# Optimization experiments

Hardware: AMD Instinct MI355X
Metric: run time of the kernel (lower is better)

The kernel has to match this reference:

```python
import jax, jax.numpy as jnp
import numpy as np

BS, D, M = 64, 256, 512


def setup_inputs() -> dict:
    key = jax.random.key(0)
    ks = jax.random.split(key, 6)
    # Small scales keep the 10-step RLS recurrence numerically stable.
    A_start = 0.05 * jax.random.normal(ks[0], (BS, D, D), dtype=jnp.float32)
    Y1 = 0.05 * jax.random.normal(ks[1], (BS, D, M), dtype=jnp.float32)
    Y2 = 0.05 * jax.random.normal(ks[2], (BS, D, M), dtype=jnp.float32)
    y1 = 0.05 * jax.random.normal(ks[3], (BS, D, 1), dtype=jnp.float32)
    y2 = 0.05 * jax.random.normal(ks[4], (BS, D, 1), dtype=jnp.float32)
    eye = jnp.broadcast_to(jnp.eye(D, dtype=jnp.float32), (BS, D, D))
    P_inv_start = 1e-3 * eye + 1e-4 * jax.random.normal(ks[5], (BS, D, D), dtype=jnp.float32)
    return {"A_start": A_start, "Y1": Y1, "Y2": Y2, "y1": y1, "y2": y2,
            "P_inv_start": P_inv_start, "h": 2, "m_prox": 10}


def _t(x):
    return jnp.swapaxes(x, 1, 2)


def reference(A_start, Y1, Y2, y1, y2, P_inv_start, h, m_prox):
    """Faithful jax version of DelayedDMD.update.

    The torch code recomputes `A_t + P_inv @ (Y1 @ (Y2^T - Y1^T @ A_t))` twice
    per step; here it is computed once (same math, fused).
    """
    Y1t, Y2t, y1t, y2t = _t(Y1), _t(Y2), _t(y1), _t(y2)
    denom = 1.0 + y1t @ P_inv_start @ y1          # (bs, 1, 1)
    Piy1 = P_inv_start @ y1                       # (bs, d, 1)

    def step(A_t, _):
        # batch recursive-least-squares prox iteration
        M_ = A_t + P_inv_start @ (Y1 @ (Y2t - Y1t @ A_t))   # (bs, d, d)
        A_new = M_ + y1 @ (y2t - y1t @ M_) / denom
        return A_new, None

    A_final_t, _ = jax.lax.scan(step, _t(A_start), None, length=m_prox)
    P_inv_new = P_inv_start - Piy1 @ (y1t @ P_inv_start) / denom
    return _t(A_final_t), P_inv_new
```

## Files before the change

kernel.cpp:

```cpp
#include <hip/hip_runtime.h>
#include <hip/hip_bf16.h>
#include <stdint.h>


#define BSZ 64
#define DD 256
#define MM 512

typedef __attribute__((ext_vector_type(8))) short short8;
typedef __attribute__((ext_vector_type(4))) float f32x4;

__device__ __forceinline__ unsigned short f2b(float f) {
    unsigned int u = __float_as_uint(f);
    unsigned int r = (u + 0x7fffu + ((u >> 16) & 1u)) >> 16;
    return (unsigned short)r;
}
__device__ __forceinline__ float b2f(unsigned short s) {
    return __uint_as_float(((unsigned int)s) << 16);
}
__device__ __forceinline__ void gll16(const void* g, void* l) {
    __builtin_amdgcn_global_load_lds(
        (const __attribute__((address_space(1))) unsigned int*)g,
        (__attribute__((address_space(3))) unsigned int*)l, 16, 0, 0);
}


__global__ __launch_bounds__(256)
void prep12(const float* __restrict__ P, const float* __restrict__ y1g,
            const float* __restrict__ Y1, const float* __restrict__ Y2,
            unsigned short* __restrict__ Pb,
            unsigned short* __restrict__ G1b, unsigned short* __restrict__ G21b,
            float* __restrict__ vec, float* __restrict__ qpart)
{
    const int blk = blockIdx.x, t = threadIdx.x;
    __shared__ __align__(16) unsigned short S[2][8192];
    __shared__ float sy1[DD];
    __shared__ float qsh[4][DD];
    if (blk >= 512) {
        const int c = blk - 512;
        const int b = c >> 3, rs = (c & 7) * 32;
        const long base = (long)b * DD * DD;
        const int wv = t >> 6, ln = t & 63;
        sy1[t] = y1g[b * DD + t];
        __syncthreads();
        const int col4 = ln * 4;
        const float4 yv = *(const float4*)(sy1 + col4);
        float4 pr[8];
#pragma unroll
        for (int i = 0; i < 8; ++i) {
            const int row = rs + i * 4 + wv;
            pr[i] = *(const float4*)(P + base + (long)row * DD + col4);
        }
        float ql0 = 0.f, ql1 = 0.f, ql2 = 0.f, ql3 = 0.f;
#pragma unroll
        for (int i = 0; i < 8; ++i) {
            const int row = rs + i * 4 + wv;
            const long o = base + (long)row * DD + col4;
            const float4 p = pr[i];
            ushort4 u;
            u.x = f2b(p.x); u.y = f2b(p.y); u.z = f2b(p.z); u.w = f2b(p.w);
            *(ushort4*)(Pb + o) = u;
            const float yr = sy1[row];
            ql0 += yr * p.x; ql1 += yr * p.y; ql2 += yr * p.z; ql3 += yr * p.w;
            float s = p.x * yv.x + p.y * yv.y + p.z * yv.z + p.w * yv.w;
#pragma unroll
            for (int off = 32; off; off >>= 1) s += __shfl_down(s, off, 64);
            if (ln == 0) vec[(long)b * 768 + row] = s;
        }
        *(float4*)(qsh[wv] + col4) = make_float4(ql0, ql1, ql2, ql3);
        __syncthreads();
        qpart[((long)c) * DD + t] = qsh[0][t] + qsh[1][t] + qsh[2][t] + qsh[3][t];
        return;
    }
    const int b = (blk & 7) + 8 * ((blk >> 3) & 7), tile = blk >> 6;
    const int i0 = (tile & 3) * 64, j0 = (tile >> 2) * 128;
    const float* A1 = Y1 + (long)b * DD * MM + (long)i0 * MM;
    const float* A2 = Y2 + (long)b * DD * MM + (long)i0 * MM;
    const float* By = Y1 + (long)b * DD * MM + (long)j0 * MM;
    const int wv = t >> 6, ln = t & 63;
    const int lr = ln & 15, qd = ln >> 4;
    const int wr = wv >> 1, wc = wv & 1;
    f32x4 acc1[2][4] = {}, acc2[2][4] = {};
    float4 fr[8];

#define P2LOAD(kc)                                                            \
    do {                                                                      \
        _Pragma("unroll")                                                     \
        for (int i = 0; i < 2; ++i) {                                         \
            const int s = i * 256 + t, row = s >> 3, c4 = s & 7;              \
            const long go = (long)row * MM + (kc) * 32 + c4 * 4;              \
            fr[i]     = *(const float4*)(A1 + go);                            \
            fr[2 + i] = *(const float4*)(A2 + go);                            \
        }                                                                     \
        _Pragma("unroll")                                                     \
        for (int i = 0; i < 4; ++i) {                                         \
            const int s = i * 256 + t, row = s >> 3, c4 = s & 7;              \
            const long go = (long)row * MM + (kc) * 32 + c4 * 4;              \
            fr[4 + i] = *(const float4*)(By + go);                            \
        }                                                                     \
    } while (0)

    P2LOAD(0);
    for (int kc = 0; kc < 16; ++kc) {
        const int u = kc & 1;
#pragma unroll
        for (int i = 0; i < 2; ++i) {
            const int s = i * 256 + t, row = s >> 3, c4 = s & 7;
            const int line = row >> 1;
            const int g8 = (((row & 1) << 2) + (c4 >> 1)) ^ (line & 7);
            const int off = line * 128 + (g8 << 4) + ((c4 & 1) << 3);
            ushort4 ua, ub;
            ua.x = f2b(fr[i].x); ua.y = f2b(fr[i].y);
            ua.z = f2b(fr[i].z); ua.w = f2b(fr[i].w);
            ub.x = f2b(fr[2 + i].x); ub.y = f2b(fr[2 + i].y);
            ub.z = f2b(fr[2 + i].z); ub.w = f2b(fr[2 + i].w);
            *(ushort4*)((char*)S[u] + off) = ua;
            *(ushort4*)((char*)S[u] + 4096 + off) = ub;
        }
#pragma unroll
        for (int i = 0; i < 4; ++i) {
            const int s = i * 256 + t, row = s >> 3, c4 = s & 7;
            const int line = row >> 1;
            const int g8 = (((row & 1) << 2) + (c4 >> 1)) ^ (line & 7);
            const int off = line * 128 + (g8 << 4) + ((c4 & 1) << 3);
            ushort4 uc;
            uc.x = f2b(fr[4 + i].x); uc.y = f2b(fr[4 + i].y);
            uc.z = f2b(fr[4 + i].z); uc.w = f2b(fr[4 + i].w);
            *(ushort4*)((char*)S[u] + 8192 + off) = uc;
        }
        __syncthreads();
        if (kc < 15) { P2LOAD(kc + 1); }
        short8 a1[2], a2[2], bfr[4];
#pragma unroll
        for (int mt = 0; mt < 2; ++mt) {
            const int row = wr * 32 + mt * 16 + lr;
            const int line = row >> 1;
            const int off = line * 128 + (((((row & 1) << 2) + qd) ^ (line & 7)) << 4);
            a1[mt] = *(const short8*)((const char*)S[u] + off);
            a2[mt] = *(const short8*)((const char*)S[u] + 4096 + off);
        }
#pragma unroll
        for (int nt = 0; nt < 4; ++nt) {
            const int row = wc * 64 + nt * 16 + lr;
            const int line = row >> 1;
            const int off = line * 128 + (((((row & 1) << 2) + qd) ^ (line & 7)) << 4);
            bfr[nt] = *(const short8*)((const char*)S[u] + 8192 + off);
        }
#pragma unroll
        for (int mt = 0; mt < 2; ++mt)
#pragma unroll
            for (int nt = 0; nt < 4; ++nt) {
                acc1[mt][nt] = __builtin_amdgcn_mfma_f32_16x16x32_bf16(
                    a1[mt], bfr[nt], acc1[mt][nt], 0, 0, 0);
                acc2[mt][nt] = __builtin_amdgcn_mfma_f32_16x16x32_bf16(
                    a2[mt], bfr[nt], acc2[mt][nt], 0, 0, 0);
            }
    }
#undef P2LOAD
    unsigned short* O1 = G1b  + (long)b * DD * DD;
    unsigned short* O2 = G21b + (long)b * DD * DD;
#pragma unroll
    for (int mt = 0; mt < 2; ++mt)
#pragma unroll
        for (int nt = 0; nt < 4; ++nt) {
            const int gr0 = i0 + wr * 32 + mt * 16 + qd * 4;
            const int gc  = j0 + wc * 64 + nt * 16 + lr;
#pragma unroll
            for (int r = 0; r < 4; ++r) {
                O1[(long)(gr0 + r) * DD + gc] = f2b(acc1[mt][nt][r]);
                O2[(long)(gr0 + r) * DD + gc] = f2b(acc2[mt][nt][r]);
            }
        }
}

__global__ __launch_bounds__(256)
void gemmEVq(const unsigned short* __restrict__ Pb, const unsigned short* __restrict__ G1b,
             const unsigned short* __restrict__ G21b,
             const float* __restrict__ y1g, const float* __restrict__ y2g,
             const float* __restrict__ vec, const float* __restrict__ qpart,
             unsigned short* __restrict__ Enb, unsigned short* __restrict__ Vpb,
             float* __restrict__ out2)
{
    __shared__ __align__(16) unsigned short S[2][2][128 * 64];
    __shared__ float qs[DD], s1[DD], s2[DD], pv[DD], red[DD];
    const int blk = blockIdx.x, t = threadIdx.x;
    const int b = (blk & 7) + 8 * (blk >> 6);
    const int rem = (blk >> 3) & 7, sel = rem >> 2, quad = rem & 3;
    const int i0 = (quad >> 1) * 128, j0 = (quad & 1) * 128;
    const char* Ab = (const char*)((sel ? G21b : Pb) + (long)b * DD * DD + (long)i0 * DD);
    const char* Bb = (const char*)((sel ? Pb : G1b) + (long)b * DD * DD + (long)j0 * DD);
    unsigned short* Ob = (sel ? Vpb : Enb) + (long)b * DD * DD;
    const int wv = t >> 6, ln = t & 63;
    const int lr = ln & 15, qd = ln >> 4;
    const int mh = (wv >> 1) * 64, nh = (wv & 1) * 64;
    const int srow = t >> 3;
    const int sc = (t & 7) * 16;

#define GEVSTAGE(u, kc)                                                           \
    _Pragma("unroll")                                                             \
    for (int i = 0; i < 4; ++i) {                                                 \
        const int row = i * 32 + srow;                                            \
        const int gco = (kc) * 128 + (sc ^ ((row & 7) << 4));                     \
        const int lo = row * 128 + sc;                                            \
        gll16(Ab + (long)row * 512 + gco, (char*)S[u][0] + lo);                   \
        gll16(Bb + (long)row * 512 + gco, (char*)S[u][1] + lo);                   \
    }

    GEVSTAGE(0, 0);
    {
        const float* qp = qpart + (long)b * 8 * DD;
        float qv = 0.f;
#pragma unroll
        for (int c = 0; c < 8; ++c) qv += qp[c * DD + t];
        qs[t] = qv;
        s1[t] = y1g[b * DD + t];
        s2[t] = y2g[b * DD + t];
        pv[t] = vec[(long)b * 768 + t];
        red[t] = pv[t] * s1[t];
        __syncthreads();
        for (int s = 128; s; s >>= 1) { if (t < s) red[t] += red[t + s]; __syncthreads(); }
    }
    const float kk = 1.0f / (1.0f + red[0]);

    f32x4 acc[4][4] = {};
    float dot[4] = {0.f, 0.f, 0.f, 0.f};

    for (int kc = 0; kc < 4; ++kc) {
        __syncthreads();
        if (kc < 3) { GEVSTAGE((kc + 1) & 1, kc + 1); }
        const unsigned short (*Su)[128 * 64] = S[kc & 1];
#pragma unroll
        for (int kc2 = 0; kc2 < 2; ++kc2) {
            const int kb = kc2 * 64 + qd * 16;
            short8 af[4], bfr[4];
#pragma unroll
            for (int mt = 0; mt < 4; ++mt) {
                const int row = mh + mt * 16 + lr;
                af[mt] = *(const short8*)((const char*)Su[0] + row * 128 +
                                          (kb ^ ((row & 7) << 4)));
            }
#pragma unroll
            for (int nt = 0; nt < 4; ++nt) {
                const int row = nh + nt * 16 + lr;
                bfr[nt] = *(const short8*)((const char*)Su[1] + row * 128 +
                                           (kb ^ ((row & 7) << 4)));
            }
            const int kel = kc * 64 + kc2 * 32 + qd * 8;
            const float4 qa = *(const float4*)(qs + kel);
            const float4 qb = *(const float4*)(qs + kel + 4);
            const float qf[8] = {qa.x, qa.y, qa.z, qa.w, qb.x, qb.y, qb.z, qb.w};
            if (!sel) {
#pragma unroll
                for (int nt = 0; nt < 4; ++nt)
#pragma unroll
                    for (int j = 0; j < 8; ++j)
                        dot[nt] += b2f((unsigned short)bfr[nt][j]) * qf[j];
            } else {
#pragma unroll
                for (int mt = 0; mt < 4; ++mt)
#pragma unroll
                    for (int j = 0; j < 8; ++j)
                        dot[mt] += b2f((unsigned short)af[mt][j]) * qf[j];
            }
#pragma unroll
            for (int mt = 0; mt < 4; ++mt)
#pragma unroll
                for (int nt = 0; nt < 4; ++nt)
                    acc[mt][nt] = __builtin_amdgcn_mfma_f32_16x16x32_bf16(
                        af[mt], bfr[nt], acc[mt][nt], 0, 0, 0);
        }
    }
#undef GEVSTAGE
#pragma unroll
    for (int i = 0; i < 4; ++i) {
        dot[i] += __shfl_xor(dot[i], 16, 64);
        dot[i] += __shfl_xor(dot[i], 32, 64);
    }
#pragma unroll
    for (int mt = 0; mt < 4; ++mt) {
#pragma unroll
        for (int nt = 0; nt < 4; ++nt) {
            const int gr0 = i0 + mh + mt * 16 + qd * 4;
            const int gc  = j0 + nh + nt * 16 + lr;
            if (!sel) {
                const float cw = s1[gc] - dot[nt];
#pragma unroll
                for (int r = 0; r < 4; ++r) {
                    const float rv = kk * s1[gr0 + r];
                    Ob[(long)(gr0 + r) * DD + gc] = f2b(-(acc[mt][nt][r] + rv * cw));
                }
            } else {
                const float cv = s1[gc];
#pragma unroll
                for (int r = 0; r < 4; ++r) {
                    const float uv = __shfl(dot[mt], qd * 4 + r, 64);
                    const float rv = kk * (s2[gr0 + r] - uv);
                    Ob[(long)(gr0 + r) * DD + gc] = f2b(acc[mt][nt][r] + rv * cv);
                }
            }
        }
    }
    {
        const long base = (long)b * DD * DD;
        const int rs = rem * 32;
#pragma unroll
        for (int i = 0; i < 8; ++i) {
            const int idx = rs * DD + (i * 256 + t) * 4;
            const int row = idx >> 8, col = idx & 255;
            const float kPi = kk * pv[row];
            const ushort4 pu = *(const ushort4*)(Pb + base + idx);
            float4 rr;
            rr.x = b2f(pu.x) - kPi * qs[col];
            rr.y = b2f(pu.y) - kPi * qs[col + 1];
            rr.z = b2f(pu.z) - kPi * qs[col + 2];
            rr.w = b2f(pu.w) - kPi * qs[col + 3];
            *(float4*)(out2 + base + idx) = rr;
        }
    }
}

__global__ __launch_bounds__(512, 4)
void iterk(const float* __restrict__ A_start, const unsigned short* __restrict__ Enb,
           const unsigned short* __restrict__ Vpb, float* __restrict__ out1)
{
    const int blk = blockIdx.x, t = threadIdx.x;
    __shared__ __align__(16) unsigned short Xsh[32 * 256];
    const int b = (blk & 7) + 8 * (blk >> 6), r0 = ((blk >> 3) & 7) * 32;
    const long base = (long)b * DD * DD;
    const float* Ab = A_start + base;
    const unsigned short* Eb = Enb + base;
    const unsigned short* Vb = Vpb + base;
    float* Ob = out1 + base;
    const int wv = t >> 6, ln = t & 63;
    const int lr = ln & 15, qd = ln >> 4;
    const int ib = wv * 32;

    f32x4 acc[2][2], vv[2][2];
    short8 ef[2][8];

#pragma unroll
    for (int it = 0; it < 2; ++it)
#pragma unroll
        for (int jt = 0; jt < 2; ++jt) {
            const long o = (long)(r0 + jt * 16 + lr) * DD + ib + it * 16 + qd * 4;
            acc[it][jt] = *(const f32x4*)(Ab + o);
            const ushort4 vu = *(const ushort4*)(Vb + o);
            vv[it][jt][0] = b2f(vu.x); vv[it][jt][1] = b2f(vu.y);
            vv[it][jt][2] = b2f(vu.z); vv[it][jt][3] = b2f(vu.w);
        }
#pragma unroll
    for (int it = 0; it < 2; ++it) {
        const long ro = (long)(ib + it * 16 + lr) * DD;
#pragma unroll
        for (int kc = 0; kc < 8; ++kc)
            ef[it][kc] = *(const short8*)(Eb + ro + kc * 32 + qd * 8);
    }

    const int gpart = wv * 4 + (qd >> 1), off8 = (qd & 1) * 8;

#pragma unroll 1
    for (int s = 0; s < 10; ++s) {
#pragma unroll
        for (int it = 0; it < 2; ++it)
#pragma unroll
            for (int jt = 0; jt < 2; ++jt) {
                const int j = jt * 16 + lr;
                const int g = (gpart + it * 2) ^ ((j & 7) << 1);
                const unsigned int p0 = (unsigned int)f2b(acc[it][jt][0]) |
                                        ((unsigned int)f2b(acc[it][jt][1]) << 16);
                const unsigned int p1 = (unsigned int)f2b(acc[it][jt][2]) |
                                        ((unsigned int)f2b(acc[it][jt][3]) << 16);
                *(uint2*)((char*)Xsh + j * 512 + g * 16 + off8) = make_uint2(p0, p1);
                acc[it][jt] += vv[it][jt];
            }
        __syncthreads();
        __builtin_amdgcn_s_setprio(1);
#pragma unroll
        for (int kc = 0; kc < 8; ++kc) {
            short8 bf[2];
#pragma unroll
            for (int jt = 0; jt < 2; ++jt) {
                const int j = jt * 16 + lr;
                const int g = (kc * 4 + qd) ^ ((j & 7) << 1);
                bf[jt] = *(const short8*)((char*)Xsh + j * 512 + g * 16);
            }
#pragma unroll
            for (int it = 0; it < 2; ++it)
#pragma unroll
                for (int jt = 0; jt < 2; ++jt)
                    acc[it][jt] = __builtin_amdgcn_mfma_f32_16x16x32_bf16(
                        ef[it][kc], bf[jt], acc[it][jt], 0, 0, 0);
        }
        __builtin_amdgcn_s_setprio(0);
        __syncthreads();
    }

#pragma unroll
    for (int it = 0; it < 2; ++it)
#pragma unroll
        for (int jt = 0; jt < 2; ++jt) {
            const long o = (long)(r0 + jt * 16 + lr) * DD + ib + it * 16 + qd * 4;
            *(f32x4*)(Ob + o) = acc[it][jt];
        }
}

extern "C" void kernel_launch(void* const* d_in, const int* in_sizes, int n_in,
                              void* d_out, int out_size, void* d_ws, size_t ws_size,
                              hipStream_t stream)
{
    const float* A_start = (const float*)d_in[0];
    const float* Y1      = (const float*)d_in[1];
    const float* Y2      = (const float*)d_in[2];
    const float* y1      = (const float*)d_in[3];
    const float* y2      = (const float*)d_in[4];
    const float* P       = (const float*)d_in[5];

    const long EL2 = (long)BSZ * DD * DD;

    float* out1 = (float*)d_out;
    float* out2 = out1 + EL2;

    char* w8 = (char*)d_ws;
    unsigned short* Pb    = (unsigned short*)(w8);
    unsigned short* G1b   = (unsigned short*)(w8 + 8388608);
    unsigned short* G21b  = (unsigned short*)(w8 + 16777216);
    unsigned short* Enb   = (unsigned short*)(w8 + 25165824);
    unsigned short* Vpb   = (unsigned short*)(w8 + 33554432);
    float*          vec   = (float*)(w8 + 41943040);
    float*          qpart = (float*)(w8 + 42139648);

    prep12<<<1024, dim3(256), 0, stream>>>(P, y1, Y1, Y2, Pb, G1b, G21b, vec, qpart);
    gemmEVq<<<512, dim3(256), 0, stream>>>(Pb, G1b, G21b, y1, y2, vec, qpart,
                                           Enb, Vpb, out2);
    iterk<<<512, dim3(512), 0, stream>>>(A_start, Enb, Vpb, out1);
}
```

Baseline: 195.4 us.

## Split prep kernel into Gram GEMM and P-conversion kernels with 512-thread GEMM blocks

Separates the heterogeneous prep kernel into a dedicated Gram-matrix GEMM kernel and a P-conversion/reduction kernel. The GEMM kernel uses 512 threads (8 waves) with smaller per-wave tiles, lowering register pressure and raising wave parallelism per tile, and adds a barrier at the end of each k-step. This costs an extra kernel launch and removes the overlap the two block types had within one grid.

```diff
diff --git a/kernel.cpp b/kernel.cpp
--- a/kernel.cpp
+++ b/kernel.cpp
@@ -25,53 +25,12 @@
 }
 
 
-__global__ __launch_bounds__(256)
-void prep12(const float* __restrict__ P, const float* __restrict__ y1g,
-            const float* __restrict__ Y1, const float* __restrict__ Y2,
-            unsigned short* __restrict__ Pb,
-            unsigned short* __restrict__ G1b, unsigned short* __restrict__ G21b,
-            float* __restrict__ vec, float* __restrict__ qpart)
+__global__ __launch_bounds__(512)
+void prepG(const float* __restrict__ Y1, const float* __restrict__ Y2,
+           unsigned short* __restrict__ G1b, unsigned short* __restrict__ G21b)
 {
+    __shared__ __align__(16) unsigned short S[2][8192];
     const int blk = blockIdx.x, t = threadIdx.x;
-    __shared__ __align__(16) unsigned short S[2][8192];
-    __shared__ float sy1[DD];
-    __shared__ float qsh[4][DD];
-    if (blk >= 512) {
-        const int c = blk - 512;
-        const int b = c >> 3, rs = (c & 7) * 32;
-        const long base = (long)b * DD * DD;
-        const int wv = t >> 6, ln = t & 63;
-        sy1[t] = y1g[b * DD + t];
-        __syncthreads();
-        const int col4 = ln * 4;
-        const float4 yv = *(const float4*)(sy1 + col4);
-        float4 pr[8];
-#pragma unroll
-        for (int i = 0; i < 8; ++i) {
-            const int row = rs + i * 4 + wv;
-            pr[i] = *(const float4*)(P + base + (long)row * DD + col4);
-        }
-        float ql0 = 0.f, ql1 = 0.f, ql2 = 0.f, ql3 = 0.f;
-#pragma unroll
-        for (int i = 0; i < 8; ++i) {
-            const int row = rs + i * 4 + wv;
-            const long o = base + (long)row * DD + col4;
-            const float4 p = pr[i];
-            ushort4 u;
-            u.x = f2b(p.x); u.y = f2b(p.y); u.z = f2b(p.z); u.w = f2b(p.w);
-            *(ushort4*)(Pb + o) = u;
-            const float yr = sy1[row];
-            ql0 += yr * p.x; ql1 += yr * p.y; ql2 += yr * p.z; ql3 += yr * p.w;
-            float s = p.x * yv.x + p.y * yv.y + p.z * yv.z + p.w * yv.w;
-#pragma unroll
-            for (int off = 32; off; off >>= 1) s += __shfl_down(s, off, 64);
-            if (ln == 0) vec[(long)b * 768 + row] = s;
-        }
-        *(float4*)(qsh[wv] + col4) = make_float4(ql0, ql1, ql2, ql3);
-        __syncthreads();
-        qpart[((long)c) * DD + t] = qsh[0][t] + qsh[1][t] + qsh[2][t] + qsh[3][t];
-        return;
-    }
     const int b = (blk & 7) + 8 * ((blk >> 3) & 7), tile = blk >> 6;
     const int i0 = (tile & 3) * 64, j0 = (tile >> 2) * 128;
     const float* A1 = Y1 + (long)b * DD * MM + (long)i0 * MM;
@@ -79,58 +38,51 @@
     const float* By = Y1 + (long)b * DD * MM + (long)j0 * MM;
     const int wv = t >> 6, ln = t & 63;
     const int lr = ln & 15, qd = ln >> 4;
-    const int wr = wv >> 1, wc = wv & 1;
-    f32x4 acc1[2][4] = {}, acc2[2][4] = {};
-    float4 fr[8];
-
-#define P2LOAD(kc)                                                            \
+    const int wr = wv >> 2, wc = wv & 3;
+    f32x4 acc1[2][2] = {}, acc2[2][2] = {};
+    float4 fa, fb, fy[2];
+
+#define PGLOAD(kc)                                                            \
     do {                                                                      \
+        const int rowA = t >> 3, c4A = t & 7;                                 \
+        const long goA = (long)rowA * MM + (kc) * 32 + c4A * 4;               \
+        fa = *(const float4*)(A1 + goA);                                      \
+        fb = *(const float4*)(A2 + goA);                                      \
         _Pragma("unroll")                                                     \
         for (int i = 0; i < 2; ++i) {                                         \
-            const int s = i * 256 + t, row = s >> 3, c4 = s & 7;              \
-            const long go = (long)row * MM + (kc) * 32 + c4 * 4;              \
-            fr[i]     = *(const float4*)(A1 + go);                            \
-            fr[2 + i] = *(const float4*)(A2 + go);                            \
-        }                                                                     \
-        _Pragma("unroll")                                                     \
-        for (int i = 0; i < 4; ++i) {                                         \
-            const int s = i * 256 + t, row = s >> 3, c4 = s & 7;              \
-            const long go = (long)row * MM + (kc) * 32 + c4 * 4;              \
-            fr[4 + i] = *(const float4*)(By + go);                            \
+            const int s = i * 512 + t, row = s >> 3, c4 = s & 7;              \
+            fy[i] = *(const float4*)(By + (long)row * MM + (kc) * 32 + c4 * 4); \
         }                                                                     \
     } while (0)
 
-    P2LOAD(0);
+    PGLOAD(0);
     for (int kc = 0; kc < 16; ++kc) {
         const int u = kc & 1;
-#pragma unroll
-        for (int i = 0; i < 2; ++i) {
-            const int s = i * 256 + t, row = s >> 3, c4 = s & 7;
+        {
+            const int row = t >> 3, c4 = t & 7;
             const int line = row >> 1;
             const int g8 = (((row & 1) << 2) + (c4 >> 1)) ^ (line & 7);
             const int off = line * 128 + (g8 << 4) + ((c4 & 1) << 3);
             ushort4 ua, ub;
-            ua.x = f2b(fr[i].x); ua.y = f2b(fr[i].y);
-            ua.z = f2b(fr[i].z); ua.w = f2b(fr[i].w);
-            ub.x = f2b(fr[2 + i].x); ub.y = f2b(fr[2 + i].y);
-            ub.z = f2b(fr[2 + i].z); ub.w = f2b(fr[2 + i].w);
+            ua.x = f2b(fa.x); ua.y = f2b(fa.y); ua.z = f2b(fa.z); ua.w = f2b(fa.w);
+            ub.x = f2b(fb.x); ub.y = f2b(fb.y); ub.z = f2b(fb.z); ub.w = f2b(fb.w);
             *(ushort4*)((char*)S[u] + off) = ua;
             *(ushort4*)((char*)S[u] + 4096 + off) = ub;
         }
 #pragma unroll
-        for (int i = 0; i < 4; ++i) {
-            const int s = i * 256 + t, row = s >> 3, c4 = s & 7;
+        for (int i = 0; i < 2; ++i) {
+            const int s = i * 512 + t, row = s >> 3, c4 = s & 7;
             const int line = row >> 1;
             const int g8 = (((row & 1) << 2) + (c4 >> 1)) ^ (line & 7);
             const int off = line * 128 + (g8 << 4) + ((c4 & 1) << 3);
             ushort4 uc;
-            uc.x = f2b(fr[4 + i].x); uc.y = f2b(fr[4 + i].y);
-            uc.z = f2b(fr[4 + i].z); uc.w = f2b(fr[4 + i].w);
+            uc.x = f2b(fy[i].x); uc.y = f2b(fy[i].y);
+            uc.z = f2b(fy[i].z); uc.w = f2b(fy[i].w);
             *(ushort4*)((char*)S[u] + 8192 + off) = uc;
         }
         __syncthreads();
-        if (kc < 15) { P2LOAD(kc + 1); }
-        short8 a1[2], a2[2], bfr[4];
+        if (kc < 15) { PGLOAD(kc + 1); }
+        short8 a1[2], a2[2], bfr[2];
 #pragma unroll
         for (int mt = 0; mt < 2; ++mt) {
             const int row = wr * 32 + mt * 16 + lr;
@@ -140,8 +92,8 @@
             a2[mt] = *(const short8*)((const char*)S[u] + 4096 + off);
         }
 #pragma unroll
-        for (int nt = 0; nt < 4; ++nt) {
-            const int row = wc * 64 + nt * 16 + lr;
+        for (int nt = 0; nt < 2; ++nt) {
+            const int row = wc * 32 + nt * 16 + lr;
             const int line = row >> 1;
             const int off = line * 128 + (((((row & 1) << 2) + qd) ^ (line & 7)) << 4);
             bfr[nt] = *(const short8*)((const char*)S[u] + 8192 + off);
@@ -149,28 +101,71 @@
 #pragma unroll
         for (int mt = 0; mt < 2; ++mt)
 #pragma unroll
-            for (int nt = 0; nt < 4; ++nt) {
+            for (int nt = 0; nt < 2; ++nt) {
                 acc1[mt][nt] = __builtin_amdgcn_mfma_f32_16x16x32_bf16(
                     a1[mt], bfr[nt], acc1[mt][nt], 0, 0, 0);
                 acc2[mt][nt] = __builtin_amdgcn_mfma_f32_16x16x32_bf16(
                     a2[mt], bfr[nt], acc2[mt][nt], 0, 0, 0);
             }
-    }
-#undef P2LOAD
+        __syncthreads();
+    }
+#undef PGLOAD
     unsigned short* O1 = G1b  + (long)b * DD * DD;
     unsigned short* O2 = G21b + (long)b * DD * DD;
 #pragma unroll
     for (int mt = 0; mt < 2; ++mt)
 #pragma unroll
-        for (int nt = 0; nt < 4; ++nt) {
+        for (int nt = 0; nt < 2; ++nt) {
             const int gr0 = i0 + wr * 32 + mt * 16 + qd * 4;
-            const int gc  = j0 + wc * 64 + nt * 16 + lr;
+            const int gc  = j0 + wc * 32 + nt * 16 + lr;
 #pragma unroll
             for (int r = 0; r < 4; ++r) {
                 O1[(long)(gr0 + r) * DD + gc] = f2b(acc1[mt][nt][r]);
                 O2[(long)(gr0 + r) * DD + gc] = f2b(acc2[mt][nt][r]);
             }
         }
+}
+
+__global__ __launch_bounds__(256)
+void prep1(const float* __restrict__ P, const float* __restrict__ y1g,
+           unsigned short* __restrict__ Pb, float* __restrict__ vec,
+           float* __restrict__ qpart)
+{
+    const int blk = blockIdx.x, t = threadIdx.x;
+    const int b = blk >> 3, rs = (blk & 7) * 32;
+    const long base = (long)b * DD * DD;
+    const int wv = t >> 6, ln = t & 63;
+    __shared__ float sy1[DD];
+    __shared__ float qsh[4][DD];
+    sy1[t] = y1g[b * DD + t];
+    __syncthreads();
+    const int col4 = ln * 4;
+    const float4 yv = *(const float4*)(sy1 + col4);
+    float4 pr[8];
+#pragma unroll
+    for (int i = 0; i < 8; ++i) {
+        const int row = rs + i * 4 + wv;
+        pr[i] = *(const float4*)(P + base + (long)row * DD + col4);
+    }
+    float ql0 = 0.f, ql1 = 0.f, ql2 = 0.f, ql3 = 0.f;
+#pragma unroll
+    for (int i = 0; i < 8; ++i) {
+        const int row = rs + i * 4 + wv;
+        const long o = base + (long)row * DD + col4;
+        const float4 p = pr[i];
+        ushort4 u;
+        u.x = f2b(p.x); u.y = f2b(p.y); u.z = f2b(p.z); u.w = f2b(p.w);
+        *(ushort4*)(Pb + o) = u;
+        const float yr = sy1[row];
+        ql0 += yr * p.x; ql1 += yr * p.y; ql2 += yr * p.z; ql3 += yr * p.w;
+        float s = p.x * yv.x + p.y * yv.y + p.z * yv.z + p.w * yv.w;
+#pragma unroll
+        for (int off = 32; off; off >>= 1) s += __shfl_down(s, off, 64);
+        if (ln == 0) vec[(long)b * 768 + row] = s;
+    }
+    *(float4*)(qsh[wv] + col4) = make_float4(ql0, ql1, ql2, ql3);
+    __syncthreads();
+    qpart[((long)blk) * DD + t] = qsh[0][t] + qsh[1][t] + qsh[2][t] + qsh[3][t];
 }
 
 __global__ __launch_bounds__(256)
@@ -429,7 +424,8 @@
     float*          vec   = (float*)(w8 + 41943040);
     float*          qpart = (float*)(w8 + 42139648);
 
-    prep12<<<1024, dim3(256), 0, stream>>>(P, y1, Y1, Y2, Pb, G1b, G21b, vec, qpart);
+    prepG<<<512, dim3(512), 0, stream>>>(Y1, Y2, G1b, G21b);
+    prep1<<<512, dim3(256), 0, stream>>>(P, y1, Pb, vec, qpart);
     gemmEVq<<<512, dim3(256), 0, stream>>>(Pb, G1b, G21b, y1, y2, vec, qpart,
                                            Enb, Vpb, out2);
     iterk<<<512, dim3(512), 0, stream>>>(A_start, Enb, Vpb, out1);
```

After: 199.9 us. +2.3%, slower.
